# Optimization experiments

Measured on AMD Instinct MI355X. Metric: run time of the kernel, lower is better.

The kernel has to match this reference:

```python
import jax, jax.numpy as jnp
import numpy as np

B, N, E = 4, 10000, 160000
D, H, HID, DE = 128, 4, 128, 16
DK = HID // H


def setup_inputs() -> dict:
    key = jax.random.key(0)
    ks = jax.random.split(key, 16)
    w = lambda k, shape: jax.random.normal(k, shape, jnp.float32) * 0.02
    return {
        "x": jax.random.normal(ks[0], (B, N, D), jnp.float32),
        "edge_index": jax.random.randint(ks[1], (2, E), 0, N, dtype=jnp.int32),
        "edge_attr": jax.random.normal(ks[2], (E, DE), jnp.float32),
        "Wq": w(ks[3], (D, HID)), "bq": jnp.zeros((HID,), jnp.float32),
        "Wk": w(ks[4], (D, HID)), "bk": jnp.zeros((HID,), jnp.float32),
        "Wv": w(ks[5], (D, HID)), "bv": jnp.zeros((HID,), jnp.float32),
        "Wf": w(ks[6], (DE, 2 * HID)), "bf": jnp.zeros((2 * HID,), jnp.float32),
        "Wo": w(ks[7], (HID, D)), "bo": jnp.zeros((D,), jnp.float32),
        "ln_g": jnp.ones((D,), jnp.float32), "ln_b": jnp.zeros((D,), jnp.float32),
    }


def reference(x, edge_index, edge_attr, Wq, bq, Wk, bk, Wv, bv, Wf, bf, Wo, bo, ln_g, ln_b):
    src, dst = edge_index[0], edge_index[1]
    # node projections -> [B, N, H, DK]
    Q = (x @ Wq + bq).reshape(B, N, H, DK)
    K = (x @ Wk + bk).reshape(B, N, H, DK)
    V = (x @ Wv + bv).reshape(B, N, H, DK)
    # edge gathers -> [B, E, H, DK]
    q_e, k_e, v_e = Q[:, dst], K[:, src], V[:, src]
    # FiLM modulation of keys (edge-conditioned, shared across batch)
    gamma, beta = jnp.split(edge_attr @ Wf + bf, 2, axis=-1)
    gamma = gamma.reshape(1, E, H, DK)
    beta = beta.reshape(1, E, H, DK)
    k_e = k_e * (1.0 + gamma) + beta
    logits = (q_e * k_e).sum(-1) / np.sqrt(DK).astype(np.float32)  # [B, E, H]

    def seg_softmax(lg):  # lg: [E, H], softmax over edges sharing a dst node
        m = jax.ops.segment_max(lg, dst, num_segments=N)       # [N, H]
        ex = jnp.exp(lg - m[dst])
        s = jax.ops.segment_sum(ex, dst, num_segments=N)        # [N, H]
        return ex / s[dst]

    att = jax.vmap(seg_softmax)(logits)                         # [B, E, H]
    msg = att[..., None] * v_e                                  # [B, E, H, DK]
    agg = jax.vmap(lambda m: jax.ops.segment_sum(m, dst, num_segments=N))(msg)
    y = agg.reshape(B, N, HID) @ Wo + bo                        # [B, N, D]
    h = x + y  # dropout is identity in eval mode
    mu = h.mean(-1, keepdims=True)
    var = ((h - mu) ** 2).mean(-1, keepdims=True)
    return (h - mu) / jnp.sqrt(var + 1e-5) * ln_g + ln_b
```

## Files before the change

### kernel.cpp

```cpp
#include <hip/hip_runtime.h>
#include <hip/hip_bf16.h>

#define B_ 4
#define N_ 10000
#define E_ 160000
#define D_ 128
#define H_ 4
#define HID_ 128
#define DK_ 32
#define DE_ 16
#define PGRID 2048

typedef __attribute__((ext_vector_type(8))) short short8v;
typedef __attribute__((ext_vector_type(4))) short short4v;
typedef __attribute__((ext_vector_type(4))) float f32x4;
typedef __attribute__((ext_vector_type(2))) float f32x2;

__device__ __forceinline__ short bfb(float f) {
  union { float f; unsigned u; } c; c.f = f;
  unsigned u = c.u + 0x7FFFu + ((c.u >> 16) & 1u);
  return (short)(u >> 16);
}
__device__ __forceinline__ float b2f(unsigned short u) {
  union { unsigned u; float f; } c; c.u = ((unsigned)u) << 16;
  return c.f;
}

__device__ __forceinline__ unsigned char f2fp8(float f) {
  int r = __builtin_amdgcn_cvt_pk_fp8_f32(f, f, 0, false);
  return (unsigned char)(r & 0xff);
}
__device__ __forceinline__ f32x2 fp8lo(unsigned u) {
  return __builtin_amdgcn_cvt_pk_f32_fp8((int)u, false);
}
__device__ __forceinline__ f32x2 fp8hi(unsigned u) {
  return __builtin_amdgcn_cvt_pk_f32_fp8((int)u, true);
}

__global__ __launch_bounds__(256) void wt_hist(
    const float* __restrict__ Wq, const float* __restrict__ Wk,
    const float* __restrict__ Wv, const float* __restrict__ Wo,
    short* __restrict__ wt, const int* __restrict__ ei,
    int* __restrict__ cnt) {
  const int blk = blockIdx.x;
  if (blk < 256) {
    const float* Ws[4] = {Wq, Wk, Wv, Wo};
    const int i = blk * 256 + threadIdx.x;
    const int m = i >> 14;
    const int k = (i >> 7) & 127;
    const int n = i & 127;
    wt[(size_t)m * 16384 + n * 128 + k] = bfb(Ws[m][k * 128 + n]);
  } else {
    const int e = (blk - 256) * 256 + threadIdx.x;
    if (e < E_) atomicAdd(&cnt[ei[E_ + e]], 1);
  }
}

__global__ __launch_bounds__(64) void qkv_mfma(
    const float* __restrict__ x, const short* __restrict__ wt,
    const float* __restrict__ bq, const float* __restrict__ bk,
    const float* __restrict__ bv,
    unsigned short* __restrict__ Qb, unsigned char* __restrict__ kv8) {
  __shared__ short xs[16][136];
  const int lane = threadIdx.x;
  const int ln15 = lane & 15;
  const int g    = lane >> 4;
  const long rowBase = (long)blockIdx.x * 16;

  for (int i = lane; i < 16 * 32; i += 64) {
    const int r  = i >> 5;
    const int c4 = (i & 31) * 4;
    const float4 v = *(const float4*)(x + (rowBase + r) * 128 + c4);
    short4v sv; sv.x = bfb(v.x); sv.y = bfb(v.y); sv.z = bfb(v.z); sv.w = bfb(v.w);
    *(short4v*)&xs[r][c4] = sv;
  }
  __syncthreads();

  short8v af[4];
#pragma unroll
  for (int kk = 0; kk < 4; ++kk)
    af[kk] = *(const short8v*)&xs[ln15][kk * 32 + g * 8];

  const float* bs[3] = {bq, bk, bv};

  int bbv[4], nnv[4];
#pragma unroll
  for (int r = 0; r < 4; ++r) {
    const long row = rowBase + g * 4 + r;
    bbv[r] = (int)(row / N_);
    nnv[r] = (int)(row - (long)bbv[r] * N_);
  }

#pragma unroll
  for (int m = 0; m < 3; ++m) {
    const short* Wt = wt + (size_t)m * 16384;
    f32x4 acc[8];
#pragma unroll
    for (int cb = 0; cb < 8; ++cb) acc[cb] = (f32x4){0.f, 0.f, 0.f, 0.f};

#pragma unroll
    for (int kk = 0; kk < 4; ++kk) {
#pragma unroll
      for (int cb = 0; cb < 8; ++cb) {
        const short8v bfr =
            *(const short8v*)(Wt + (cb * 16 + ln15) * 128 + kk * 32 + g * 8);
        acc[cb] = __builtin_amdgcn_mfma_f32_16x16x32_bf16(af[kk], bfr, acc[cb], 0, 0, 0);
      }
    }

    const float* bias = bs[m];
#pragma unroll
    for (int cb = 0; cb < 8; ++cb) {
      const int col = cb * 16 + ln15;
      const float bv_ = bias[col];
#pragma unroll
      for (int r = 0; r < 4; ++r) {
        const float val = acc[cb][r] + bv_;
        if (m == 0) {
          const long row = rowBase + g * 4 + r;
          Qb[row * 128 + col] = (unsigned short)bfb(val);
        } else {
          kv8[(((size_t)nnv[r] * 4 + bbv[r]) << 8) + (m - 1) * 128 + col] = f2fp8(val);
        }
      }
    }
  }
}

__global__ __launch_bounds__(1024) void csr_scan(const int* __restrict__ cnt,
                                                 int* __restrict__ rowptr,
                                                 int* __restrict__ fill) {
  __shared__ int part[1024];
  const int t = threadIdx.x;
  int local[10];
  int sum = 0;
#pragma unroll
  for (int i = 0; i < 10; ++i) {
    const int idx = t * 10 + i;
    local[i] = sum;
    sum += (idx < N_) ? cnt[idx] : 0;
  }
  part[t] = sum;
  __syncthreads();
  for (int off = 1; off < 1024; off <<= 1) {
    const int v = (t >= off) ? part[t - off] : 0;
    __syncthreads();
    part[t] += v;
    __syncthreads();
  }
  const int excl = (t == 0) ? 0 : part[t - 1];
#pragma unroll
  for (int i = 0; i < 10; ++i) {
    const int idx = t * 10 + i;
    if (idx <= N_) {
      const int o = excl + local[i];
      rowptr[idx] = o;
      if (idx < N_) fill[idx] = o;
    }
  }
}

__global__ __launch_bounds__(256) void csr_scatter(
    const int* __restrict__ ei, int* __restrict__ fill,
    int* __restrict__ esrc, int* __restrict__ eord) {
  const int e = blockIdx.x * 256 + threadIdx.x;
  if (e < E_) {
    const int dst = ei[E_ + e];
    const int pos = atomicAdd(&fill[dst], 1);
    esrc[pos] = ei[e];
    eord[pos] = e;
  }
}

__global__ __launch_bounds__(256) void film_prep(
    const float* __restrict__ ea, const float* __restrict__ Wf,
    const float* __restrict__ bf, unsigned char* __restrict__ film8) {
  const int lane = threadIdx.x & 63;
  const int wave = threadIdx.x >> 6;
  const int c0 = lane * 4;

  float4 w[16];
#pragma unroll
  for (int j = 0; j < 16; ++j) w[j] = *(const float4*)(Wf + j * 256 + c0);
  const float4 bias = *(const float4*)(bf + c0);

  for (int i = blockIdx.x * 4 + wave; i < E_; i += PGRID * 4) {
    const float* ep = ea + (size_t)i * 16;
    const float4 a0 = *(const float4*)ep;
    const float4 a1 = *(const float4*)(ep + 4);
    const float4 a2 = *(const float4*)(ep + 8);
    const float4 a3 = *(const float4*)(ep + 12);
    const float ev[16] = {a0.x,a0.y,a0.z,a0.w, a1.x,a1.y,a1.z,a1.w,
                          a2.x,a2.y,a2.z,a2.w, a3.x,a3.y,a3.z,a3.w};
    float ox = bias.x, oy = bias.y, oz = bias.z, ow = bias.w;
#pragma unroll
    for (int j = 0; j < 16; ++j) {
      ox = fmaf(ev[j], w[j].x, ox);
      oy = fmaf(ev[j], w[j].y, oy);
      oz = fmaf(ev[j], w[j].z, oz);
      ow = fmaf(ev[j], w[j].w, ow);
    }
    int r = __builtin_amdgcn_cvt_pk_fp8_f32(ox, oy, 0, false);
    r = __builtin_amdgcn_cvt_pk_fp8_f32(oz, ow, r, true);
    ((int*)(film8 + (size_t)i * 256))[lane] = r;
  }
}

__global__ __launch_bounds__(256) void fused_attn(
    const int* __restrict__ rowptr, const int* __restrict__ esrc,
    const int* __restrict__ eord, const unsigned char* __restrict__ film8,
    const unsigned short* __restrict__ Qb,
    const unsigned char* __restrict__ kv8, float* __restrict__ agg) {
  const int wave = threadIdx.x >> 6;
  const int lane = threadIdx.x & 63;
  const int e2 = lane >> 5;
  const int dh = (lane >> 4) & 1;
  const int b  = (lane >> 2) & 3;
  const int h  = lane & 3;
  const int col0 = h * 32 + dh * 16;

  for (int node = blockIdx.x * 4 + wave; node < N_; node += PGRID * 4) {
    const int beg = rowptr[node], end = rowptr[node + 1];

    float q[16];
    {
      const unsigned short* qp = Qb + ((size_t)b * N_ + node) * 128 + col0;
      const short8v t0 = *(const short8v*)qp;
      const short8v t1 = *(const short8v*)(qp + 8);
#pragma unroll
      for (int j = 0; j < 8; ++j) {
        q[j]     = b2f((unsigned short)t0[j]);
        q[8 + j] = b2f((unsigned short)t1[j]);
      }
    }
    float acc[16];
#pragma unroll
    for (int d = 0; d < 16; ++d) acc[d] = 0.f;
    float se = 0.f;

    for (int i0 = beg; i0 < end; i0 += 2) {
      const int ii = i0 + e2;
      const bool valid = ii < end;
      const int ic = valid ? ii : i0;
      const int src = esrc[ic];
      const int de  = eord[ic];
      const unsigned char* kp = kv8 + ((((size_t)src << 2) + b) << 8) + col0;
      const unsigned char* fp = film8 + (size_t)de * 256 + col0;
      const uint4 kw = *(const uint4*)kp;
      const uint4 vw = *(const uint4*)(kp + 128);
      const uint4 gw = *(const uint4*)fp;
      const uint4 tw = *(const uint4*)(fp + 128);
      const unsigned ks[4] = {kw.x, kw.y, kw.z, kw.w};
      const unsigned vs[4] = {vw.x, vw.y, vw.z, vw.w};
      const unsigned gs[4] = {gw.x, gw.y, gw.z, gw.w};
      const unsigned ts[4] = {tw.x, tw.y, tw.z, tw.w};

      float pacc[4] = {0.f, 0.f, 0.f, 0.f};
#pragma unroll
      for (int w = 0; w < 4; ++w) {
        const f32x2 k0 = fp8lo(ks[w]), k1 = fp8hi(ks[w]);
        const f32x2 g0 = fp8lo(gs[w]), g1 = fp8hi(gs[w]);
        const f32x2 t0 = fp8lo(ts[w]), t1 = fp8hi(ts[w]);
        float km;
        km = k0.x + fmaf(k0.x, g0.x, t0.x); pacc[w] = fmaf(q[4*w+0], km, pacc[w]);
        km = k0.y + fmaf(k0.y, g0.y, t0.y); pacc[w] = fmaf(q[4*w+1], km, pacc[w]);
        km = k1.x + fmaf(k1.x, g1.x, t1.x); pacc[w] = fmaf(q[4*w+2], km, pacc[w]);
        km = k1.y + fmaf(k1.y, g1.y, t1.y); pacc[w] = fmaf(q[4*w+3], km, pacc[w]);
      }
      float pl = (pacc[0] + pacc[1]) + (pacc[2] + pacc[3]);
      pl += __shfl_xor(pl, 16);

      float ex = __expf(pl * 0.17677669529663687f);
      ex = valid ? ex : 0.f;
      se += ex;
#pragma unroll
      for (int w = 0; w < 4; ++w) {
        const f32x2 v0 = fp8lo(vs[w]), v1 = fp8hi(vs[w]);
        acc[4*w+0] = fmaf(ex, v0.x, acc[4*w+0]);
        acc[4*w+1] = fmaf(ex, v0.y, acc[4*w+1]);
        acc[4*w+2] = fmaf(ex, v1.x, acc[4*w+2]);
        acc[4*w+3] = fmaf(ex, v1.y, acc[4*w+3]);
      }
    }

#pragma unroll
    for (int d = 0; d < 16; ++d) acc[d] += __shfl_xor(acc[d], 32);
    se += __shfl_xor(se, 32);

    if (e2 == 0) {
      const float inv = (end > beg) ? 1.f / se : 0.f;
      float* ap = agg + ((size_t)b * N_ + node) * 128 + col0;
#pragma unroll
      for (int c = 0; c < 4; ++c) {
        float4 o;
        o.x = acc[c*4+0] * inv; o.y = acc[c*4+1] * inv;
        o.z = acc[c*4+2] * inv; o.w = acc[c*4+3] * inv;
        *(float4*)(ap + c * 4) = o;
      }
    }
  }
}

__global__ __launch_bounds__(64) void out_ln_mfma(
    const float* __restrict__ agg, const short* __restrict__ wto,
    const float* __restrict__ bo, const float* __restrict__ x,
    const float* __restrict__ lng, const float* __restrict__ lnb,
    float* __restrict__ out) {
  __shared__ short as_[16][136];
  const int lane = threadIdx.x;
  const int ln15 = lane & 15;
  const int g    = lane >> 4;
  const long rowBase = (long)blockIdx.x * 16;

  for (int i = lane; i < 16 * 32; i += 64) {
    const int r  = i >> 5;
    const int c4 = (i & 31) * 4;
    const float4 v = *(const float4*)(agg + (rowBase + r) * 128 + c4);
    short4v sv; sv.x = bfb(v.x); sv.y = bfb(v.y); sv.z = bfb(v.z); sv.w = bfb(v.w);
    *(short4v*)&as_[r][c4] = sv;
  }
  __syncthreads();

  short8v af[4];
#pragma unroll
  for (int kk = 0; kk < 4; ++kk)
    af[kk] = *(const short8v*)&as_[ln15][kk * 32 + g * 8];

  f32x4 acc[8];
#pragma unroll
  for (int cb = 0; cb < 8; ++cb) acc[cb] = (f32x4){0.f, 0.f, 0.f, 0.f};

#pragma unroll
  for (int kk = 0; kk < 4; ++kk) {
#pragma unroll
    for (int cb = 0; cb < 8; ++cb) {
      const short8v bfr =
          *(const short8v*)(wto + (cb * 16 + ln15) * 128 + kk * 32 + g * 8);
      acc[cb] = __builtin_amdgcn_mfma_f32_16x16x32_bf16(af[kk], bfr, acc[cb], 0, 0, 0);
    }
  }

#pragma unroll
  for (int cb = 0; cb < 8; ++cb) {
    const int col = cb * 16 + ln15;
    const float bov = bo[col];
#pragma unroll
    for (int r = 0; r < 4; ++r) {
      const long row = rowBase + g * 4 + r;
      acc[cb][r] += bov + x[row * 128 + col];
    }
  }

  float s1[4], s2[4];
#pragma unroll
  for (int r = 0; r < 4; ++r) {
    s1[r] = 0.f; s2[r] = 0.f;
#pragma unroll
    for (int cb = 0; cb < 8; ++cb) {
      s1[r] += acc[cb][r];
      s2[r] = fmaf(acc[cb][r], acc[cb][r], s2[r]);
    }
  }
#pragma unroll
  for (int m = 1; m < 16; m <<= 1) {
#pragma unroll
    for (int r = 0; r < 4; ++r) {
      s1[r] += __shfl_xor(s1[r], m);
      s2[r] += __shfl_xor(s2[r], m);
    }
  }
  float mu[4], inv[4];
#pragma unroll
  for (int r = 0; r < 4; ++r) {
    mu[r] = s1[r] * (1.f / 128.f);
    const float var = s2[r] * (1.f / 128.f) - mu[r] * mu[r];
    inv[r] = rsqrtf(var + 1e-5f);
  }

#pragma unroll
  for (int cb = 0; cb < 8; ++cb) {
    const int col = cb * 16 + ln15;
    const float gv = lng[col], bv_ = lnb[col];
#pragma unroll
    for (int r = 0; r < 4; ++r) {
      const long row = rowBase + g * 4 + r;
      out[row * 128 + col] = (acc[cb][r] - mu[r]) * inv[r] * gv + bv_;
    }
  }
}

extern "C" void kernel_launch(void* const* d_in, const int* in_sizes, int n_in,
                              void* d_out, int out_size, void* d_ws, size_t ws_size,
                              hipStream_t stream) {
  const float* x   = (const float*)d_in[0];
  const int*   ei  = (const int*)d_in[1];
  const float* ea  = (const float*)d_in[2];
  const float* Wq  = (const float*)d_in[3];
  const float* bq  = (const float*)d_in[4];
  const float* Wk  = (const float*)d_in[5];
  const float* bk  = (const float*)d_in[6];
  const float* Wv  = (const float*)d_in[7];
  const float* bv  = (const float*)d_in[8];
  const float* Wf  = (const float*)d_in[9];
  const float* bf  = (const float*)d_in[10];
  const float* Wo  = (const float*)d_in[11];
  const float* bo  = (const float*)d_in[12];
  const float* lng = (const float*)d_in[13];
  const float* lnb = (const float*)d_in[14];
  float* out = (float*)d_out;

  const size_t NQ = (size_t)B_ * N_ * HID_;

  char* base = (char*)d_ws;
  size_t off = 0;
  unsigned short* Qb = (unsigned short*)(base + off); off += NQ * 2;
  float* agg  = (float*)(base + off); off += NQ * 4;
  unsigned char* kv8 = (unsigned char*)(base + off);
  off += (size_t)B_ * N_ * 256;
  unsigned char* film8 = (unsigned char*)(base + off);
  off += (size_t)E_ * 256;
  short* wt   = (short*)(base + off); off += 4 * 16384 * 2;
  int*  cnt    = (int*)(base + off); off += N_ * 4;
  int*  rowptr = (int*)(base + off); off += (N_ + 1) * 4;
  int*  fill   = (int*)(base + off); off += N_ * 4;
  int*  esrc   = (int*)(base + off); off += E_ * 4;
  int*  eord   = (int*)(base + off); off += E_ * 4;

  hipMemsetAsync(cnt, 0, N_ * sizeof(int), stream);

  wt_hist<<<256 + (E_ + 255) / 256, 256, 0, stream>>>(Wq, Wk, Wv, Wo, wt, ei, cnt);
  qkv_mfma<<<(B_ * N_) / 16, 64, 0, stream>>>(x, wt, bq, bk, bv, Qb, kv8);
  csr_scan<<<1, 1024, 0, stream>>>(cnt, rowptr, fill);
  csr_scatter<<<(E_ + 255) / 256, 256, 0, stream>>>(ei, fill, esrc, eord);
  film_prep<<<PGRID, 256, 0, stream>>>(ea, Wf, bf, film8);
  fused_attn<<<PGRID, 256, 0, stream>>>(rowptr, esrc, eord, film8, Qb, kv8, agg);
  out_ln_mfma<<<(B_ * N_) / 16, 64, 0, stream>>>(agg, wt + 3 * 16384, bo, x, lng, lnb, out);
}
```

Measured before the change: 171.5 us.

## Merge QKV projection, FiLM prep and degree histogram into one launch

The QKV MFMA projection, the FiLM edge-modulation precompute and the destination-degree histogram now run as a single kernel whose blocks split by index range into three roles. The weight transpose stays in its own small kernel. QKV blocks now hold four waves each (256 threads) instead of one, and FiLM uses a smaller grid with a longer stride loop. The goal is fewer launches and letting the independent stages overlap on the GPU. In exchange, the blocks are heterogeneous and the QKV part uses more shared memory per block.

```diff
diff --git a/kernel.cpp b/kernel.cpp
--- a/kernel.cpp
+++ b/kernel.cpp
@@ -10,6 +10,9 @@
 #define DK_ 32
 #define DE_ 16
 #define PGRID 2048
+#define QKV_BLKS 625
+#define FILM_BLKS 512
+#define HIST_BLKS 625
 
 typedef __attribute__((ext_vector_type(8))) short short8v;
 typedef __attribute__((ext_vector_type(4))) short short4v;
@@ -37,93 +40,128 @@
   return __builtin_amdgcn_cvt_pk_f32_fp8((int)u, true);
 }
 
-__global__ __launch_bounds__(256) void wt_hist(
+__global__ __launch_bounds__(256) void wt_prep(
     const float* __restrict__ Wq, const float* __restrict__ Wk,
     const float* __restrict__ Wv, const float* __restrict__ Wo,
-    short* __restrict__ wt, const int* __restrict__ ei,
-    int* __restrict__ cnt) {
-  const int blk = blockIdx.x;
-  if (blk < 256) {
-    const float* Ws[4] = {Wq, Wk, Wv, Wo};
-    const int i = blk * 256 + threadIdx.x;
-    const int m = i >> 14;
-    const int k = (i >> 7) & 127;
-    const int n = i & 127;
-    wt[(size_t)m * 16384 + n * 128 + k] = bfb(Ws[m][k * 128 + n]);
-  } else {
-    const int e = (blk - 256) * 256 + threadIdx.x;
-    if (e < E_) atomicAdd(&cnt[ei[E_ + e]], 1);
-  }
-}
-
-__global__ __launch_bounds__(64) void qkv_mfma(
+    short* __restrict__ wt) {
+  const float* Ws[4] = {Wq, Wk, Wv, Wo};
+  const int i = blockIdx.x * 256 + threadIdx.x;
+  const int m = i >> 14;
+  const int k = (i >> 7) & 127;
+  const int n = i & 127;
+  wt[(size_t)m * 16384 + n * 128 + k] = bfb(Ws[m][k * 128 + n]);
+}
+
+__global__ __launch_bounds__(256) void phase1(
     const float* __restrict__ x, const short* __restrict__ wt,
     const float* __restrict__ bq, const float* __restrict__ bk,
     const float* __restrict__ bv,
-    unsigned short* __restrict__ Qb, unsigned char* __restrict__ kv8) {
-  __shared__ short xs[16][136];
-  const int lane = threadIdx.x;
-  const int ln15 = lane & 15;
-  const int g    = lane >> 4;
-  const long rowBase = (long)blockIdx.x * 16;
-
-  for (int i = lane; i < 16 * 32; i += 64) {
-    const int r  = i >> 5;
-    const int c4 = (i & 31) * 4;
-    const float4 v = *(const float4*)(x + (rowBase + r) * 128 + c4);
-    short4v sv; sv.x = bfb(v.x); sv.y = bfb(v.y); sv.z = bfb(v.z); sv.w = bfb(v.w);
-    *(short4v*)&xs[r][c4] = sv;
-  }
-  __syncthreads();
-
-  short8v af[4];
-#pragma unroll
-  for (int kk = 0; kk < 4; ++kk)
-    af[kk] = *(const short8v*)&xs[ln15][kk * 32 + g * 8];
-
-  const float* bs[3] = {bq, bk, bv};
-
-  int bbv[4], nnv[4];
-#pragma unroll
-  for (int r = 0; r < 4; ++r) {
-    const long row = rowBase + g * 4 + r;
-    bbv[r] = (int)(row / N_);
-    nnv[r] = (int)(row - (long)bbv[r] * N_);
-  }
-
-#pragma unroll
-  for (int m = 0; m < 3; ++m) {
-    const short* Wt = wt + (size_t)m * 16384;
-    f32x4 acc[8];
-#pragma unroll
-    for (int cb = 0; cb < 8; ++cb) acc[cb] = (f32x4){0.f, 0.f, 0.f, 0.f};
-
-#pragma unroll
-    for (int kk = 0; kk < 4; ++kk) {
+    unsigned short* __restrict__ Qb, unsigned char* __restrict__ kv8,
+    const float* __restrict__ ea, const float* __restrict__ Wf,
+    const float* __restrict__ bf, unsigned char* __restrict__ film8,
+    const int* __restrict__ ei, int* __restrict__ cnt) {
+  const int blk = blockIdx.x;
+
+  if (blk < QKV_BLKS) {
+    __shared__ short xs[4][16][136];
+    const int wave = threadIdx.x >> 6;
+    const int lane = threadIdx.x & 63;
+    const int ln15 = lane & 15;
+    const int g    = lane >> 4;
+    const long rowBase = ((long)blk * 4 + wave) * 16;
+
+    for (int i = lane; i < 16 * 32; i += 64) {
+      const int r  = i >> 5;
+      const int c4 = (i & 31) * 4;
+      const float4 v = *(const float4*)(x + (rowBase + r) * 128 + c4);
+      short4v sv; sv.x = bfb(v.x); sv.y = bfb(v.y); sv.z = bfb(v.z); sv.w = bfb(v.w);
+      *(short4v*)&xs[wave][r][c4] = sv;
+    }
+    __syncthreads();
+
+    short8v af[4];
+#pragma unroll
+    for (int kk = 0; kk < 4; ++kk)
+      af[kk] = *(const short8v*)&xs[wave][ln15][kk * 32 + g * 8];
+
+    const float* bs[3] = {bq, bk, bv};
+
+    int bbv[4], nnv[4];
+#pragma unroll
+    for (int r = 0; r < 4; ++r) {
+      const long row = rowBase + g * 4 + r;
+      bbv[r] = (int)(row / N_);
+      nnv[r] = (int)(row - (long)bbv[r] * N_);
+    }
+
+#pragma unroll
+    for (int m = 0; m < 3; ++m) {
+      const short* Wt = wt + (size_t)m * 16384;
+      f32x4 acc[8];
+#pragma unroll
+      for (int cb = 0; cb < 8; ++cb) acc[cb] = (f32x4){0.f, 0.f, 0.f, 0.f};
+
+#pragma unroll
+      for (int kk = 0; kk < 4; ++kk) {
+#pragma unroll
+        for (int cb = 0; cb < 8; ++cb) {
+          const short8v bfr =
+              *(const short8v*)(Wt + (cb * 16 + ln15) * 128 + kk * 32 + g * 8);
+          acc[cb] = __builtin_amdgcn_mfma_f32_16x16x32_bf16(af[kk], bfr, acc[cb], 0, 0, 0);
+        }
+      }
+
+      const float* bias = bs[m];
 #pragma unroll
       for (int cb = 0; cb < 8; ++cb) {
-        const short8v bfr =
-            *(const short8v*)(Wt + (cb * 16 + ln15) * 128 + kk * 32 + g * 8);
-        acc[cb] = __builtin_amdgcn_mfma_f32_16x16x32_bf16(af[kk], bfr, acc[cb], 0, 0, 0);
-      }
-    }
-
-    const float* bias = bs[m];
-#pragma unroll
-    for (int cb = 0; cb < 8; ++cb) {
-      const int col = cb * 16 + ln15;
-      const float bv_ = bias[col];
-#pragma unroll
-      for (int r = 0; r < 4; ++r) {
-        const float val = acc[cb][r] + bv_;
-        if (m == 0) {
-          const long row = rowBase + g * 4 + r;
-          Qb[row * 128 + col] = (unsigned short)bfb(val);
-        } else {
-          kv8[(((size_t)nnv[r] * 4 + bbv[r]) << 8) + (m - 1) * 128 + col] = f2fp8(val);
+        const int col = cb * 16 + ln15;
+        const float bv_ = bias[col];
+#pragma unroll
+        for (int r = 0; r < 4; ++r) {
+          const float val = acc[cb][r] + bv_;
+          if (m == 0) {
+            const long row = rowBase + g * 4 + r;
+            Qb[row * 128 + col] = (unsigned short)bfb(val);
+          } else {
+            kv8[(((size_t)nnv[r] * 4 + bbv[r]) << 8) + (m - 1) * 128 + col] = f2fp8(val);
+          }
         }
       }
     }
+  } else if (blk < QKV_BLKS + FILM_BLKS) {
+    const int fb   = blk - QKV_BLKS;
+    const int lane = threadIdx.x & 63;
+    const int wave = threadIdx.x >> 6;
+    const int c0 = lane * 4;
+
+    float4 w[16];
+#pragma unroll
+    for (int j = 0; j < 16; ++j) w[j] = *(const float4*)(Wf + j * 256 + c0);
+    const float4 bias = *(const float4*)(bf + c0);
+
+    for (int i = fb * 4 + wave; i < E_; i += FILM_BLKS * 4) {
+      const float* ep = ea + (size_t)i * 16;
+      const float4 a0 = *(const float4*)ep;
+      const float4 a1 = *(const float4*)(ep + 4);
+      const float4 a2 = *(const float4*)(ep + 8);
+      const float4 a3 = *(const float4*)(ep + 12);
+      const float ev[16] = {a0.x,a0.y,a0.z,a0.w, a1.x,a1.y,a1.z,a1.w,
+                            a2.x,a2.y,a2.z,a2.w, a3.x,a3.y,a3.z,a3.w};
+      float ox = bias.x, oy = bias.y, oz = bias.z, ow = bias.w;
+#pragma unroll
+      for (int j = 0; j < 16; ++j) {
+        ox = fmaf(ev[j], w[j].x, ox);
+        oy = fmaf(ev[j], w[j].y, oy);
+        oz = fmaf(ev[j], w[j].z, oz);
+        ow = fmaf(ev[j], w[j].w, ow);
+      }
+      int r = __builtin_amdgcn_cvt_pk_fp8_f32(ox, oy, 0, false);
+      r = __builtin_amdgcn_cvt_pk_fp8_f32(oz, ow, r, true);
+      ((int*)(film8 + (size_t)i * 256))[lane] = r;
+    }
+  } else {
+    const int e = (blk - QKV_BLKS - FILM_BLKS) * 256 + threadIdx.x;
+    if (e < E_) atomicAdd(&cnt[ei[E_ + e]], 1);
   }
 }
 
@@ -169,40 +207,6 @@
     const int pos = atomicAdd(&fill[dst], 1);
     esrc[pos] = ei[e];
     eord[pos] = e;
-  }
-}
-
-__global__ __launch_bounds__(256) void film_prep(
-    const float* __restrict__ ea, const float* __restrict__ Wf,
-    const float* __restrict__ bf, unsigned char* __restrict__ film8) {
-  const int lane = threadIdx.x & 63;
-  const int wave = threadIdx.x >> 6;
-  const int c0 = lane * 4;
-
-  float4 w[16];
-#pragma unroll
-  for (int j = 0; j < 16; ++j) w[j] = *(const float4*)(Wf + j * 256 + c0);
-  const float4 bias = *(const float4*)(bf + c0);
-
-  for (int i = blockIdx.x * 4 + wave; i < E_; i += PGRID * 4) {
-    const float* ep = ea + (size_t)i * 16;
-    const float4 a0 = *(const float4*)ep;
-    const float4 a1 = *(const float4*)(ep + 4);
-    const float4 a2 = *(const float4*)(ep + 8);
-    const float4 a3 = *(const float4*)(ep + 12);
-    const float ev[16] = {a0.x,a0.y,a0.z,a0.w, a1.x,a1.y,a1.z,a1.w,
-                          a2.x,a2.y,a2.z,a2.w, a3.x,a3.y,a3.z,a3.w};
-    float ox = bias.x, oy = bias.y, oz = bias.z, ow = bias.w;
-#pragma unroll
-    for (int j = 0; j < 16; ++j) {
-      ox = fmaf(ev[j], w[j].x, ox);
-      oy = fmaf(ev[j], w[j].y, oy);
-      oz = fmaf(ev[j], w[j].z, oz);
-      ow = fmaf(ev[j], w[j].w, ow);
-    }
-    int r = __builtin_amdgcn_cvt_pk_fp8_f32(ox, oy, 0, false);
-    r = __builtin_amdgcn_cvt_pk_fp8_f32(oz, ow, r, true);
-    ((int*)(film8 + (size_t)i * 256))[lane] = r;
   }
 }
 
@@ -428,11 +432,11 @@
 
   hipMemsetAsync(cnt, 0, N_ * sizeof(int), stream);
 
-  wt_hist<<<256 + (E_ + 255) / 256, 256, 0, stream>>>(Wq, Wk, Wv, Wo, wt, ei, cnt);
-  qkv_mfma<<<(B_ * N_) / 16, 64, 0, stream>>>(x, wt, bq, bk, bv, Qb, kv8);
+  wt_prep<<<256, 256, 0, stream>>>(Wq, Wk, Wv, Wo, wt);
+  phase1<<<QKV_BLKS + FILM_BLKS + HIST_BLKS, 256, 0, stream>>>(
+      x, wt, bq, bk, bv, Qb, kv8, ea, Wf, bf, film8, ei, cnt);
   csr_scan<<<1, 1024, 0, stream>>>(cnt, rowptr, fill);
   csr_scatter<<<(E_ + 255) / 256, 256, 0, stream>>>(ei, fill, esrc, eord);
-  film_prep<<<PGRID, 256, 0, stream>>>(ea, Wf, bf, film8);
   fused_attn<<<PGRID, 256, 0, stream>>>(rowptr, esrc, eord, film8, Qb, kv8, agg);
   out_ln_mfma<<<(B_ * N_) / 16, 64, 0, stream>>>(agg, wt + 3 * 16384, bo, x, lng, lnb, out);
 }
```

Result: no change. 173.4 us (+1.1%).
